# Kernel tuning notes

Measured on AMD Instinct MI355X. Metric: run time of the kernel, lower is better.

Reference implementation:

```python
import jax, jax.numpy as jnp
import numpy as np

KH, KW = 3, 3  # window_size[1], window_size[2]
FILTERS = 64
CHANNELS = 32
K = KH * KW * CHANNELS


def _extract_patches_valid(x, kh, kw):
    # TF tf.image.extract_patches ordering: (row_offset, col_offset, channel)
    B, H, W, C = x.shape
    Ho, Wo = H - kh + 1, W - kw + 1
    cols = [x[:, i:i + Ho, j:j + Wo, :] for i in range(kh) for j in range(kw)]
    return jnp.concatenate(cols, axis=-1)  # (B, Ho, Wo, kh*kw*C)


def setup_inputs() -> dict:
    key = jax.random.key(0)
    kx, kw = jax.random.split(key)
    x = jax.random.normal(kx, (8, 32, 32, CHANNELS), dtype=jnp.float32)
    # learned weight per __init__: shape (1, 1, 1, K, filters), random_normal init
    w = jax.random.normal(kw, (1, 1, 1, K, FILTERS), dtype=jnp.float32) * 0.05
    return {"x": x, "w": w}


def reference(x, w):
    # patches: (B, Ho, Wo, K)
    patches = _extract_patches_valid(x, KH, KW)
    # broadcast-add against weights: (B, Ho, Wo, K, filters)
    s = patches[..., None] + w[0, 0, 0]  # w[0,0,0]: (K, filters)
    # tropical conv: max over patch axis minus min over patch axis
    return jnp.max(s, axis=3) - jnp.min(s, axis=3)  # (B, Ho, Wo, filters)
```

## Files before the change

kernel.cpp:

```cpp
#include <hip/hip_runtime.h>


#define C_IN 32
#define NF 64
#define H_OUT 30
#define W_OUT 30
#define W_IN 32

__global__ __launch_bounds__(256) void tropconv_kernel(
    const float* __restrict__ x,
    const float* __restrict__ w,
    float* __restrict__ out) {
    const int bx = blockIdx.x;
    const int q = bx & 3;
    const int bho = bx >> 2;
    const int b = bho / H_OUT;
    const int ho = bho - b * H_OUT;
    const int tid = threadIdx.x;
    const int lane = tid & 63;
    const int wave = tid >> 6;

    const int col0 = q * 8;
    const int npx = (q == 3) ? 6 : 8;
    const int ncols = (q == 3) ? 8 : 10;

    __shared__ float xs[3 * 10 * C_IN];
    __shared__ float pmx[4][8][NF];
    __shared__ float pmn[4][8][NF];

    {
        const int nf4_row = ncols * (C_IN / 4);
        const int total_f4 = 3 * nf4_row;
        if (tid < total_f4) {
            const int r = tid / nf4_row;
            const int cc = tid - r * nf4_row;
            const float4* __restrict__ src = (const float4*)(
                x + ((size_t)((b * 32 + ho + r) * W_IN + col0)) * C_IN);
            ((float4*)xs)[r * 80 + cc] = src[cc];
        }
    }
    __syncthreads();

    float mx[8], mn[8];
    #pragma unroll
    for (int t = 0; t < 8; ++t) { mx[t] = -INFINITY; mn[t] = INFINITY; }

    for (int ij = 0; ij < 9; ++ij) {
        const int i = ij / 3;
        const int j = ij - i * 3;

        float wreg[8];
        const float* __restrict__ wp =
            w + ((size_t)(ij * C_IN + wave * 8)) * NF + lane;
        #pragma unroll
        for (int cc = 0; cc < 8; ++cc) wreg[cc] = wp[cc * NF];

        #pragma unroll
        for (int px = 0; px < 8; ++px) {
            if (px < npx) {
                const float* __restrict__ pp =
                    xs + (i * 10 + (px + j)) * C_IN + wave * 8;
                float4 p0 = ((const float4*)pp)[0];
                float4 p1 = ((const float4*)pp)[1];
                float s0 = p0.x + wreg[0];
                float s1 = p0.y + wreg[1];
                float s2 = p0.z + wreg[2];
                float s3 = p0.w + wreg[3];
                float s4 = p1.x + wreg[4];
                float s5 = p1.y + wreg[5];
                float s6 = p1.z + wreg[6];
                float s7 = p1.w + wreg[7];
                float hi = fmaxf(fmaxf(fmaxf(s0, s1), fmaxf(s2, s3)),
                                 fmaxf(fmaxf(s4, s5), fmaxf(s6, s7)));
                float lo = fminf(fminf(fminf(s0, s1), fminf(s2, s3)),
                                 fminf(fminf(s4, s5), fminf(s6, s7)));
                mx[px] = fmaxf(mx[px], hi);
                mn[px] = fminf(mn[px], lo);
            }
        }
    }

    #pragma unroll
    for (int px = 0; px < 8; ++px) {
        pmx[wave][px][lane] = mx[px];
        pmn[wave][px][lane] = mn[px];
    }
    __syncthreads();

    const int nout = npx * NF;
    for (int e = tid; e < nout; e += 256) {
        const int px = e >> 6;
        const int f = e & 63;
        float a = fmaxf(fmaxf(pmx[0][px][f], pmx[1][px][f]),
                        fmaxf(pmx[2][px][f], pmx[3][px][f]));
        float m = fminf(fminf(pmn[0][px][f], pmn[1][px][f]),
                        fminf(pmn[2][px][f], pmn[3][px][f]));
        out[((size_t)bho * W_OUT + (col0 + px)) * NF + f] = a - m;
    }
}

extern "C" void kernel_launch(void* const* d_in, const int* in_sizes, int n_in,
                              void* d_out, int out_size, void* d_ws, size_t ws_size,
                              hipStream_t stream) {
    const float* x = (const float*)d_in[0];
    const float* w = (const float*)d_in[1];
    float* out = (float*)d_out;

    dim3 grid(8 * H_OUT * 4);
    dim3 block(256);
    tropconv_kernel<<<grid, block, 0, stream>>>(x, w, out);
}
```

Before: 64.89 us.

## Split channels across eight waves and prefetch next weight slice

Doubles the block to 512 threads, so each of 8 waves handles 4 input channels instead of 8. The cross-wave reduction in shared memory grows to 8 partials. Weights for the next kernel offset are prefetched into registers while the current offset is being computed, and the per-pixel npx guard is removed so the inner loop is fully unrolled. Max/min are written as 3-input forms so the compiler can emit max3/min3. The aim is more latency hiding and less serial work per thread. The cost is a larger reduction, more shared memory, and reads of unloaded shared-memory columns for the last column group, whose results are discarded.

```diff
diff --git a/kernel.cpp b/kernel.cpp
--- a/kernel.cpp
+++ b/kernel.cpp
@@ -7,7 +7,14 @@
 #define W_OUT 30
 #define W_IN 32
 
-__global__ __launch_bounds__(256) void tropconv_kernel(
+static __device__ __forceinline__ float max3f(float a, float b, float c) {
+    return fmaxf(fmaxf(a, b), c);
+}
+static __device__ __forceinline__ float min3f(float a, float b, float c) {
+    return fminf(fminf(a, b), c);
+}
+
+__global__ __launch_bounds__(512) void tropconv_kernel(
     const float* __restrict__ x,
     const float* __restrict__ w,
     float* __restrict__ out) {
@@ -24,9 +31,9 @@
     const int npx = (q == 3) ? 6 : 8;
     const int ncols = (q == 3) ? 8 : 10;
 
-    __shared__ float xs[3 * 10 * C_IN];
-    __shared__ float pmx[4][8][NF];
-    __shared__ float pmn[4][8][NF];
+    __shared__ __align__(16) float xs[3 * 10 * C_IN];
+    __shared__ float pmx[8][8][NF];
+    __shared__ float pmn[8][8][NF];
 
     {
         const int nf4_row = ncols * (C_IN / 4);
@@ -39,45 +46,45 @@
             ((float4*)xs)[r * 80 + cc] = src[cc];
         }
     }
+
+    const float* __restrict__ wbase = w + (size_t)(wave * 4) * NF + lane;
+
+    float wc[4];
+    #pragma unroll
+    for (int cc = 0; cc < 4; ++cc) wc[cc] = wbase[cc * NF];
+
     __syncthreads();
 
     float mx[8], mn[8];
     #pragma unroll
     for (int t = 0; t < 8; ++t) { mx[t] = -INFINITY; mn[t] = INFINITY; }
 
+    #pragma unroll
     for (int ij = 0; ij < 9; ++ij) {
+        float wn[4];
+        if (ij < 8) {
+            #pragma unroll
+            for (int cc = 0; cc < 4; ++cc)
+                wn[cc] = wbase[((ij + 1) * C_IN + cc) * NF];
+        }
+
         const int i = ij / 3;
         const int j = ij - i * 3;
-
-        float wreg[8];
-        const float* __restrict__ wp =
-            w + ((size_t)(ij * C_IN + wave * 8)) * NF + lane;
-        #pragma unroll
-        for (int cc = 0; cc < 8; ++cc) wreg[cc] = wp[cc * NF];
+        const float* __restrict__ xrow = xs + (i * 10 + j) * C_IN + wave * 4;
 
         #pragma unroll
         for (int px = 0; px < 8; ++px) {
-            if (px < npx) {
-                const float* __restrict__ pp =
-                    xs + (i * 10 + (px + j)) * C_IN + wave * 8;
-                float4 p0 = ((const float4*)pp)[0];
-                float4 p1 = ((const float4*)pp)[1];
-                float s0 = p0.x + wreg[0];
-                float s1 = p0.y + wreg[1];
-                float s2 = p0.z + wreg[2];
-                float s3 = p0.w + wreg[3];
-                float s4 = p1.x + wreg[4];
-                float s5 = p1.y + wreg[5];
-                float s6 = p1.z + wreg[6];
-                float s7 = p1.w + wreg[7];
-                float hi = fmaxf(fmaxf(fmaxf(s0, s1), fmaxf(s2, s3)),
-                                 fmaxf(fmaxf(s4, s5), fmaxf(s6, s7)));
-                float lo = fminf(fminf(fminf(s0, s1), fminf(s2, s3)),
-                                 fminf(fminf(s4, s5), fminf(s6, s7)));
-                mx[px] = fmaxf(mx[px], hi);
-                mn[px] = fminf(mn[px], lo);
-            }
+            float4 p = *(const float4*)(xrow + px * C_IN);
+            float s0 = p.x + wc[0];
+            float s1 = p.y + wc[1];
+            float s2 = p.z + wc[2];
+            float s3 = p.w + wc[3];
+            mx[px] = max3f(max3f(s0, s1, s2), s3, mx[px]);
+            mn[px] = min3f(min3f(s0, s1, s2), s3, mn[px]);
         }
+
+        #pragma unroll
+        for (int cc = 0; cc < 4; ++cc) wc[cc] = wn[cc];
     }
 
     #pragma unroll
@@ -88,13 +95,17 @@
     __syncthreads();
 
     const int nout = npx * NF;
-    for (int e = tid; e < nout; e += 256) {
-        const int px = e >> 6;
-        const int f = e & 63;
-        float a = fmaxf(fmaxf(pmx[0][px][f], pmx[1][px][f]),
-                        fmaxf(pmx[2][px][f], pmx[3][px][f]));
-        float m = fminf(fminf(pmn[0][px][f], pmn[1][px][f]),
-                        fminf(pmn[2][px][f], pmn[3][px][f]));
+    if (tid < nout) {
+        const int px = tid >> 6;
+        const int f = tid & 63;
+        float a = fmaxf(fmaxf(fmaxf(pmx[0][px][f], pmx[1][px][f]),
+                              fmaxf(pmx[2][px][f], pmx[3][px][f])),
+                        fmaxf(fmaxf(pmx[4][px][f], pmx[5][px][f]),
+                              fmaxf(pmx[6][px][f], pmx[7][px][f])));
+        float m = fminf(fminf(fminf(pmn[0][px][f], pmn[1][px][f]),
+                              fminf(pmn[2][px][f], pmn[3][px][f])),
+                        fminf(fminf(pmn[4][px][f], pmn[5][px][f]),
+                              fminf(pmn[6][px][f], pmn[7][px][f])));
         out[((size_t)bho * W_OUT + (col0 + px)) * NF + f] = a - m;
     }
 }
@@ -107,6 +118,6 @@
     float* out = (float*)d_out;
 
     dim3 grid(8 * H_OUT * 4);
-    dim3 block(256);
+    dim3 block(512);
     tropconv_kernel<<<grid, block, 0, stream>>>(x, w, out);
 }
```

New measurement: 63.29 us. 1.03x faster.
